# Performance work log

Measured on AMD Instinct MI355X. Metric: run time of the kernel, lower is better.

Reference implementation:

```python
import jax, jax.numpy as jnp
import numpy as np

B, S, D, H = 2, 2048, 1024, 16
HD = D // H


def setup_inputs() -> dict:
    key = jax.random.key(0)
    ks = jax.random.split(key, 9)
    std = 0.02
    return {
        "x": jax.random.normal(ks[0], (B, S, D), dtype=jnp.float32),
        "wq": jax.random.normal(ks[1], (D, D), dtype=jnp.float32) * std,
        "bq": jnp.zeros((D,), dtype=jnp.float32),
        "wk": jax.random.normal(ks[2], (D, D), dtype=jnp.float32) * std,
        "bk": jnp.zeros((D,), dtype=jnp.float32),
        "wv": jax.random.normal(ks[3], (D, D), dtype=jnp.float32) * std,
        "bv": jnp.zeros((D,), dtype=jnp.float32),
        "wo": jax.random.normal(ks[4], (D, D), dtype=jnp.float32) * std,
        "bo": jnp.zeros((D,), dtype=jnp.float32),
    }


def reference(x, wq, bq, wk, bk, wv, bv, wo, bo):
    bsz, seq_len, d_model = x.shape
    # projections: torch Linear computes x @ W.T + b with W of shape (out, in)
    q = (x @ wq.T + bq).reshape(bsz, seq_len, H, HD).transpose(0, 2, 1, 3)  # bhsd
    k = (x @ wk.T + bk).reshape(bsz, seq_len, H, HD).transpose(0, 2, 1, 3)
    v = (x @ wv.T + bv).reshape(bsz, seq_len, H, HD).transpose(0, 2, 1, 3)
    scale = HD ** -0.5
    scores = jnp.einsum("bhqd,bhkd->bhqk", q, k) * scale  # [B,H,S,S]
    causal = jnp.tril(jnp.ones((seq_len, seq_len), dtype=bool))
    scores = jnp.where(causal[None, None], scores, -jnp.inf)
    attn = jax.nn.softmax(scores, axis=-1)
    ctx = jnp.einsum("bhqk,bhkd->bhqd", attn, v)
    ctx = ctx.transpose(0, 2, 1, 3).reshape(bsz, seq_len, d_model)
    return ctx @ wo.T + bo
```

## Files before the change

kernel.cpp:

```cpp
#include <hip/hip_runtime.h>
#include <hip/hip_bf16.h>

#define B_  2
#define S_  2048
#define D_  1024
#define H_  16
#define HD_ 64
#define M_  (B_ * S_)

typedef __bf16 bf16;
typedef __bf16 bf16x4 __attribute__((ext_vector_type(4)));
typedef __bf16 bf16x8 __attribute__((ext_vector_type(8)));
typedef float  f32x4  __attribute__((ext_vector_type(4)));

__device__ __forceinline__ bf16x8 ld8g(const bf16* p) { return *(const bf16x8*)p; }

#define GLL(g, l) __builtin_amdgcn_global_load_lds( \
    (const __attribute__((address_space(1))) void*)(g), \
    (__attribute__((address_space(3))) void*)(l), 16, 0, 0)

__global__ __launch_bounds__(256) void convert_kernel(
    const float* __restrict__ x,  const float* __restrict__ wq,
    const float* __restrict__ wk, const float* __restrict__ wv,
    const float* __restrict__ wo,
    bf16* __restrict__ xb,  bf16* __restrict__ wqb, bf16* __restrict__ wkb,
    bf16* __restrict__ wvb, bf16* __restrict__ wob)
{
    const int seg = blockIdx.y;
    const float* src;
    bf16* dst;
    if (seg < 4)      { src = x  + (long)seg * 1048576; dst = xb  + (long)seg * 1048576; }
    else if (seg == 4){ src = wq; dst = wqb; }
    else if (seg == 5){ src = wk; dst = wkb; }
    else if (seg == 6){ src = wv; dst = wvb; }
    else              { src = wo; dst = wob; }
    const long i = ((long)blockIdx.x * 256 + threadIdx.x) * 8;
    float4 a = *(const float4*)(src + i);
    float4 b = *(const float4*)(src + i + 4);
    bf16x8 r;
    r[0] = (bf16)a.x; r[1] = (bf16)a.y; r[2] = (bf16)a.z; r[3] = (bf16)a.w;
    r[4] = (bf16)b.x; r[5] = (bf16)b.y; r[6] = (bf16)b.z; r[7] = (bf16)b.w;
    *(bf16x8*)(dst + i) = r;
}

__device__ __forceinline__ void gemm_acc_bk32(
    const bf16* __restrict__ A, const bf16* __restrict__ Bt,
    f32x4 (&acc)[4][4])
{
    __shared__ bf16 As[128 * 32];
    __shared__ bf16 Bs[128 * 32];

    const int tid  = threadIdx.x;
    const int wave = tid >> 6;
    const int lane = tid & 63;
    const int quad = lane >> 4;
    const int l15  = lane & 15;
    const int wr   = (wave >> 1) * 64;
    const int wc   = (wave & 1) * 64;
    const int m0   = blockIdx.y * 128;
    const int n0   = blockIdx.x * 128;

    const int sr = wave * 16 + (lane >> 2);
    const int sc = (lane & 3) * 8;
    const bf16* Ag = A  + (long)(m0 + sr) * D_ + sc;
    const bf16* Bg = Bt + (long)(n0 + sr) * D_ + sc;
    bf16* lA = As + wave * 512;
    bf16* lB = Bs + wave * 512;

    for (int k0 = 0; k0 < D_; k0 += 32) {
        __syncthreads();
        GLL(Ag + k0,             lA);
        GLL(Ag + 64 * D_ + k0,   lA + 64 * 32);
        GLL(Bg + k0,             lB);
        GLL(Bg + 64 * D_ + k0,   lB + 64 * 32);
        __syncthreads();

        bf16x8 af[4], bfr[4];
        for (int mi = 0; mi < 4; mi++)
            af[mi] = *(const bf16x8*)&As[(wr + mi * 16 + l15) * 32 + quad * 8];
        for (int ni = 0; ni < 4; ni++)
            bfr[ni] = *(const bf16x8*)&Bs[(wc + ni * 16 + l15) * 32 + quad * 8];

        for (int mi = 0; mi < 4; mi++)
            for (int ni = 0; ni < 4; ni++)
                acc[mi][ni] = __builtin_amdgcn_mfma_f32_16x16x32_bf16(
                    af[mi], bfr[ni], acc[mi][ni], 0, 0, 0);
    }
}

__global__ __launch_bounds__(256) void gemm_qkv(
    const bf16* __restrict__ xb,
    const bf16* __restrict__ wqb, const bf16* __restrict__ wkb, const bf16* __restrict__ wvb,
    const float* __restrict__ bq, const float* __restrict__ bk, const float* __restrict__ bv,
    bf16* __restrict__ qb, bf16* __restrict__ kb, bf16* __restrict__ vt)
{
    const bf16*  Bt   = (blockIdx.z == 0) ? wqb : (blockIdx.z == 1) ? wkb : wvb;
    const float* bias = (blockIdx.z == 0) ? bq  : (blockIdx.z == 1) ? bk  : bv;

    f32x4 acc[4][4] = {};
    gemm_acc_bk32(xb, Bt, acc);

    const int lane = threadIdx.x & 63;
    const int wave = threadIdx.x >> 6;
    const int quad = lane >> 4;
    const int l15  = lane & 15;
    const int wr   = (wave >> 1) * 64;
    const int wc   = (wave & 1) * 64;
    const int m0   = blockIdx.y * 128;
    const int n0   = blockIdx.x * 128;

    if (blockIdx.z < 2) {
        bf16* Cout = (blockIdx.z == 0) ? qb : kb;
        for (int ni = 0; ni < 4; ni++) {
            const int col = n0 + wc + ni * 16 + l15;
            const float bv = bias[col];
            for (int mi = 0; mi < 4; mi++) {
                const int rowb = m0 + wr + mi * 16 + quad * 4;
                for (int r = 0; r < 4; r++)
                    Cout[(long)(rowb + r) * D_ + col] = (bf16)(acc[mi][ni][r] + bv);
            }
        }
    } else {
        for (int ni = 0; ni < 4; ni++) {
            const int col = n0 + wc + ni * 16 + l15;
            const float bv = bias[col];
            const int h = col >> 6, hd = col & (HD_ - 1);
            for (int mi = 0; mi < 4; mi++) {
                const int rowb = m0 + wr + mi * 16 + quad * 4;
                const int b = rowb >> 11;
                const int s0 = rowb & (S_ - 1);
                bf16x4 v4;
                for (int r = 0; r < 4; r++) v4[r] = (bf16)(acc[mi][ni][r] + bv);
                *(bf16x4*)&vt[(((long)(b * H_ + h)) * HD_ + hd) * S_ + s0] = v4;
            }
        }
    }
}

__global__ __launch_bounds__(256) void gemm_out(
    const bf16* __restrict__ cb, const bf16* __restrict__ wob,
    const float* __restrict__ bo, float* __restrict__ out)
{
    f32x4 acc[4][4] = {};
    gemm_acc_bk32(cb, wob, acc);

    const int lane = threadIdx.x & 63;
    const int wave = threadIdx.x >> 6;
    const int quad = lane >> 4;
    const int l15  = lane & 15;
    const int wr   = (wave >> 1) * 64;
    const int wc   = (wave & 1) * 64;
    const int m0   = blockIdx.y * 128;
    const int n0   = blockIdx.x * 128;

    for (int ni = 0; ni < 4; ni++) {
        const int col = n0 + wc + ni * 16 + l15;
        const float bv = bo[col];
        for (int mi = 0; mi < 4; mi++) {
            const int rowb = m0 + wr + mi * 16 + quad * 4;
            for (int r = 0; r < 4; r++)
                out[(long)(rowb + r) * D_ + col] = acc[mi][ni][r] + bv;
        }
    }
}

__global__ __launch_bounds__(512) void attn_kernel(
    const bf16* __restrict__ Q, const bf16* __restrict__ K,
    const bf16* __restrict__ vt, bf16* __restrict__ ctx)
{
    constexpr int LDK = 72;
    __shared__ bf16 Ks[2][64 * LDK];
    __shared__ bf16 Vt[2][64 * LDK];
    __shared__ bf16 Pq[8][16 * LDK];

    const int tid  = threadIdx.x;
    const int wave = tid >> 6;
    const int lane = tid & 63;
    const int quad = lane >> 4;
    const int l15  = lane & 15;
    const int bh   = blockIdx.y;
    const int qt   = (blockIdx.y < 16) ? blockIdx.x : (15 - (int)blockIdx.x);
    const int b    = bh >> 4, h = bh & 15;
    const long base  = ((long)b * S_) * D_ + h * HD_;
    const bf16* Vth  = vt + (long)bh * HD_ * S_;

    const int krow = tid >> 3;
    const int kcol = (tid & 7) * 8;

    const int qw    = qt * 128 + wave * 16;
    const int qrow  = qw + l15;
    const bf16* Qr = Q + base + (long)qrow * D_;
    bf16x8 qf0 = ld8g(&Qr[quad * 8]);
    bf16x8 qf1 = ld8g(&Qr[quad * 8 + 32]);

    float l_i = 0.f;
    f32x4 o_acc[4] = {};

    auto process_tile = [&](int kbase, int buf) {
        if (kbase > qw + 15) return;
        f32x4 sc[4];
        for (int kt = 0; kt < 4; kt++) {
            const bf16* Kr = &Ks[buf][(kt * 16 + l15) * LDK + quad * 8];
            bf16x8 a0 = *(const bf16x8*)Kr;
            bf16x8 a1 = *(const bf16x8*)(Kr + 32);
            f32x4 z = {};
            z = __builtin_amdgcn_mfma_f32_16x16x32_bf16(a0, qf0, z, 0, 0, 0);
            z = __builtin_amdgcn_mfma_f32_16x16x32_bf16(a1, qf1, z, 0, 0, 0);
            sc[kt] = z;
        }
        float sum = 0.f;
        if (kbase + 63 > qw) {
            for (int kt = 0; kt < 4; kt++)
                for (int r = 0; r < 4; r++) {
                    const int k_g = kbase + kt * 16 + quad * 4 + r;
                    const float p = (k_g <= qrow) ? __expf(sc[kt][r] * 0.125f) : 0.f;
                    sc[kt][r] = p;
                    sum += p;
                }
        } else {
            for (int kt = 0; kt < 4; kt++)
                for (int r = 0; r < 4; r++) {
                    const float p = __expf(sc[kt][r] * 0.125f);
                    sc[kt][r] = p;
                    sum += p;
                }
        }
        sum += __shfl_xor(sum, 16, 64);
        sum += __shfl_xor(sum, 32, 64);
        l_i += sum;

        bf16* Pw = &Pq[wave][0];
        for (int kt = 0; kt < 4; kt++) {
            union { uint2 u; bf16 hh[4]; } pk;
            pk.hh[0] = (bf16)sc[kt][0];
            pk.hh[1] = (bf16)sc[kt][1];
            pk.hh[2] = (bf16)sc[kt][2];
            pk.hh[3] = (bf16)sc[kt][3];
            *(uint2*)&Pw[l15 * LDK + kt * 16 + quad * 4] = pk.u;
        }
        __asm__ volatile("s_waitcnt lgkmcnt(0)" ::: "memory");
        bf16x8 pf0 = *(const bf16x8*)&Pw[l15 * LDK + quad * 8];
        bf16x8 pf1 = *(const bf16x8*)&Pw[l15 * LDK + quad * 8 + 32];

        for (int ni = 0; ni < 4; ni++) {
            const bf16* Vr = &Vt[buf][(ni * 16 + l15) * LDK + quad * 8];
            bf16x8 av0 = *(const bf16x8*)Vr;
            bf16x8 av1 = *(const bf16x8*)(Vr + 32);
            o_acc[ni] = __builtin_amdgcn_mfma_f32_16x16x32_bf16(av0, pf0, o_acc[ni], 0, 0, 0);
            o_acc[ni] = __builtin_amdgcn_mfma_f32_16x16x32_bf16(av1, pf1, o_acc[ni], 0, 0, 0);
        }
    };

    bf16x8 kA = ld8g(K + base + (long)krow * D_ + kcol);
    bf16x8 wA = ld8g(Vth + (long)krow * S_ + kcol);
    bf16x8 kB = ld8g(K + base + (long)(64 + krow) * D_ + kcol);
    bf16x8 wB = ld8g(Vth + (long)krow * S_ + 64 + kcol);

    const int njt = 2 * qt + 2;
    for (int j = 0; j < njt; j += 2) {
        __syncthreads();
        *(bf16x8*)&Ks[0][krow * LDK + kcol] = kA;
        *(bf16x8*)&Vt[0][krow * LDK + kcol] = wA;
        *(bf16x8*)&Ks[1][krow * LDK + kcol] = kB;
        *(bf16x8*)&Vt[1][krow * LDK + kcol] = wB;
        if (j + 2 < njt) {
            kA = ld8g(K + base + (long)((j + 2) * 64 + krow) * D_ + kcol);
            wA = ld8g(Vth + (long)krow * S_ + (j + 2) * 64 + kcol);
            kB = ld8g(K + base + (long)((j + 3) * 64 + krow) * D_ + kcol);
            wB = ld8g(Vth + (long)krow * S_ + (j + 3) * 64 + kcol);
        }
        __syncthreads();
        process_tile(j * 64, 0);
        process_tile(j * 64 + 64, 1);
    }

    const float invl = 1.f / l_i;
    bf16* Pw = &Pq[wave][0];
    for (int ni = 0; ni < 4; ni++)
        for (int r = 0; r < 4; r++)
            Pw[l15 * LDK + ni * 16 + quad * 4 + r] = (bf16)(o_acc[ni][r] * invl);
    __asm__ volatile("s_waitcnt lgkmcnt(0)" ::: "memory");
    for (int round = 0; round < 2; round++) {
        const int rowq = (lane >> 3) + round * 8;
        bf16x8 val = *(const bf16x8*)&Pw[rowq * LDK + (lane & 7) * 8];
        const int q_g = qt * 128 + wave * 16 + rowq;
        *(bf16x8*)&ctx[base + (long)q_g * D_ + (lane & 7) * 8] = val;
    }
}

extern "C" void kernel_launch(void* const* d_in, const int* in_sizes, int n_in,
                              void* d_out, int out_size, void* d_ws, size_t ws_size,
                              hipStream_t stream)
{
    const float* x  = (const float*)d_in[0];
    const float* wq = (const float*)d_in[1];
    const float* bq = (const float*)d_in[2];
    const float* wk = (const float*)d_in[3];
    const float* bk = (const float*)d_in[4];
    const float* wv = (const float*)d_in[5];
    const float* bv = (const float*)d_in[6];
    const float* wo = (const float*)d_in[7];
    const float* bo = (const float*)d_in[8];
    float* out = (float*)d_out;

    const long NX = (long)M_ * D_;
    const long NW = (long)D_ * D_;
    bf16* xb  = (bf16*)d_ws;
    bf16* wqb = xb  + NX;
    bf16* wkb = wqb + NW;
    bf16* wvb = wkb + NW;
    bf16* wob = wvb + NW;
    bf16* qb  = wob + NW;
    bf16* kb  = qb  + NX;
    bf16* vt  = kb  + NX;
    bf16* cb  = xb;

    dim3 blk(256, 1, 1);

    convert_kernel<<<dim3(512, 8), blk, 0, stream>>>(
        x, wq, wk, wv, wo, xb, wqb, wkb, wvb, wob);

    gemm_qkv<<<dim3(8, 32, 3), blk, 0, stream>>>(
        xb, wqb, wkb, wvb, bq, bk, bv, qb, kb, vt);

    attn_kernel<<<dim3(16, 32), dim3(512, 1, 1), 0, stream>>>(qb, kb, vt, cb);

    gemm_out<<<dim3(8, 32), blk, 0, stream>>>(cb, wob, bo, out);
}
```

Before: 183.2 us.

## Process two query sub-tiles per wave in attention and shrink output GEMM tile

Result: no change. 185.4 us (+1.2%).

```diff
diff --git a/kernel.cpp b/kernel.cpp
--- a/kernel.cpp
+++ b/kernel.cpp
@@ -141,22 +141,50 @@
     const bf16* __restrict__ cb, const bf16* __restrict__ wob,
     const float* __restrict__ bo, float* __restrict__ out)
 {
-    f32x4 acc[4][4] = {};
-    gemm_acc_bk32(cb, wob, acc);
-
-    const int lane = threadIdx.x & 63;
-    const int wave = threadIdx.x >> 6;
+    __shared__ bf16 As[64 * 32];
+    __shared__ bf16 Bs[128 * 32];
+
+    const int tid  = threadIdx.x;
+    const int wave = tid >> 6;
+    const int lane = tid & 63;
     const int quad = lane >> 4;
     const int l15  = lane & 15;
-    const int wr   = (wave >> 1) * 64;
+    const int wr   = (wave >> 1) * 32;
     const int wc   = (wave & 1) * 64;
-    const int m0   = blockIdx.y * 128;
+    const int m0   = blockIdx.y * 64;
     const int n0   = blockIdx.x * 128;
+
+    const int sr = tid >> 2;
+    const int scg = (tid & 3) * 8;
+    const bf16* Ag = cb  + (long)(m0 + sr) * D_ + scg;
+    const bf16* Bg = wob + (long)(n0 + sr) * D_ + scg;
+    bf16* lA = As + wave * 512;
+    bf16* lB = Bs + wave * 512;
+
+    f32x4 acc[2][4] = {};
+    for (int k0 = 0; k0 < D_; k0 += 32) {
+        __syncthreads();
+        GLL(Ag + k0,            lA);
+        GLL(Bg + k0,            lB);
+        GLL(Bg + 64 * D_ + k0,  lB + 64 * 32);
+        __syncthreads();
+
+        bf16x8 af[2], bfr[4];
+        for (int mi = 0; mi < 2; mi++)
+            af[mi] = *(const bf16x8*)&As[(wr + mi * 16 + l15) * 32 + quad * 8];
+        for (int ni = 0; ni < 4; ni++)
+            bfr[ni] = *(const bf16x8*)&Bs[(wc + ni * 16 + l15) * 32 + quad * 8];
+
+        for (int mi = 0; mi < 2; mi++)
+            for (int ni = 0; ni < 4; ni++)
+                acc[mi][ni] = __builtin_amdgcn_mfma_f32_16x16x32_bf16(
+                    af[mi], bfr[ni], acc[mi][ni], 0, 0, 0);
+    }
 
     for (int ni = 0; ni < 4; ni++) {
         const int col = n0 + wc + ni * 16 + l15;
         const float bv = bo[col];
-        for (int mi = 0; mi < 4; mi++) {
+        for (int mi = 0; mi < 2; mi++) {
             const int rowb = m0 + wr + mi * 16 + quad * 4;
             for (int r = 0; r < 4; r++)
                 out[(long)(rowb + r) * D_ + col] = acc[mi][ni][r] + bv;
@@ -164,14 +192,14 @@
     }
 }
 
-__global__ __launch_bounds__(512) void attn_kernel(
+__global__ __launch_bounds__(256) void attn_kernel(
     const bf16* __restrict__ Q, const bf16* __restrict__ K,
     const bf16* __restrict__ vt, bf16* __restrict__ ctx)
 {
     constexpr int LDK = 72;
     __shared__ bf16 Ks[2][64 * LDK];
     __shared__ bf16 Vt[2][64 * LDK];
-    __shared__ bf16 Pq[8][16 * LDK];
+    __shared__ bf16 Pq[4][32 * LDK];
 
     const int tid  = threadIdx.x;
     const int wave = tid >> 6;
@@ -184,106 +212,170 @@
     const long base  = ((long)b * S_) * D_ + h * HD_;
     const bf16* Vth  = vt + (long)bh * HD_ * S_;
 
-    const int krow = tid >> 3;
-    const int kcol = (tid & 7) * 8;
-
-    const int qw    = qt * 128 + wave * 16;
-    const int qrow  = qw + l15;
-    const bf16* Qr = Q + base + (long)qrow * D_;
-    bf16x8 qf0 = ld8g(&Qr[quad * 8]);
-    bf16x8 qf1 = ld8g(&Qr[quad * 8 + 32]);
-
-    float l_i = 0.f;
-    f32x4 o_acc[4] = {};
+    const int r0 = tid >> 3;
+    const int c0 = (tid & 7) * 8;
+
+    const int qw    = qt * 128 + wave * 32;
+    const int qrow0 = qw + l15;
+    const int qrow1 = qw + 16 + l15;
+    const bf16* Qr0 = Q + base + (long)qrow0 * D_;
+    const bf16* Qr1 = Q + base + (long)qrow1 * D_;
+    bf16x8 qf00 = ld8g(&Qr0[quad * 8]);
+    bf16x8 qf01 = ld8g(&Qr0[quad * 8 + 32]);
+    bf16x8 qf10 = ld8g(&Qr1[quad * 8]);
+    bf16x8 qf11 = ld8g(&Qr1[quad * 8 + 32]);
+
+    float l0 = 0.f, l1 = 0.f;
+    f32x4 o0[4] = {}, o1[4] = {};
 
     auto process_tile = [&](int kbase, int buf) {
-        if (kbase > qw + 15) return;
-        f32x4 sc[4];
+        if (kbase > qw + 31) return;
+        f32x4 s0[4], s1[4];
+        __builtin_amdgcn_s_setprio(1);
+        #pragma unroll
         for (int kt = 0; kt < 4; kt++) {
             const bf16* Kr = &Ks[buf][(kt * 16 + l15) * LDK + quad * 8];
             bf16x8 a0 = *(const bf16x8*)Kr;
             bf16x8 a1 = *(const bf16x8*)(Kr + 32);
-            f32x4 z = {};
-            z = __builtin_amdgcn_mfma_f32_16x16x32_bf16(a0, qf0, z, 0, 0, 0);
-            z = __builtin_amdgcn_mfma_f32_16x16x32_bf16(a1, qf1, z, 0, 0, 0);
-            sc[kt] = z;
-        }
-        float sum = 0.f;
+            f32x4 z0 = {}, z1 = {};
+            z0 = __builtin_amdgcn_mfma_f32_16x16x32_bf16(a0, qf00, z0, 0, 0, 0);
+            z0 = __builtin_amdgcn_mfma_f32_16x16x32_bf16(a1, qf01, z0, 0, 0, 0);
+            z1 = __builtin_amdgcn_mfma_f32_16x16x32_bf16(a0, qf10, z1, 0, 0, 0);
+            z1 = __builtin_amdgcn_mfma_f32_16x16x32_bf16(a1, qf11, z1, 0, 0, 0);
+            s0[kt] = z0; s1[kt] = z1;
+        }
+        __builtin_amdgcn_s_setprio(0);
+
+        float sum0 = 0.f, sum1 = 0.f;
         if (kbase + 63 > qw) {
+            #pragma unroll
             for (int kt = 0; kt < 4; kt++)
+                #pragma unroll
                 for (int r = 0; r < 4; r++) {
                     const int k_g = kbase + kt * 16 + quad * 4 + r;
-                    const float p = (k_g <= qrow) ? __expf(sc[kt][r] * 0.125f) : 0.f;
-                    sc[kt][r] = p;
-                    sum += p;
+                    const float p = (k_g <= qrow0) ? __expf(s0[kt][r] * 0.125f) : 0.f;
+                    s0[kt][r] = p;
+                    sum0 += p;
                 }
         } else {
+            #pragma unroll
             for (int kt = 0; kt < 4; kt++)
+                #pragma unroll
                 for (int r = 0; r < 4; r++) {
-                    const float p = __expf(sc[kt][r] * 0.125f);
-                    sc[kt][r] = p;
-                    sum += p;
+                    const float p = __expf(s0[kt][r] * 0.125f);
+                    s0[kt][r] = p;
+                    sum0 += p;
                 }
         }
-        sum += __shfl_xor(sum, 16, 64);
-        sum += __shfl_xor(sum, 32, 64);
-        l_i += sum;
+        if (kbase + 63 > qw + 16) {
+            #pragma unroll
+            for (int kt = 0; kt < 4; kt++)
+                #pragma unroll
+                for (int r = 0; r < 4; r++) {
+                    const int k_g = kbase + kt * 16 + quad * 4 + r;
+                    const float p = (k_g <= qrow1) ? __expf(s1[kt][r] * 0.125f) : 0.f;
+                    s1[kt][r] = p;
+                    sum1 += p;
+                }
+        } else {
+            #pragma unroll
+            for (int kt = 0; kt < 4; kt++)
+                #pragma unroll
+                for (int r = 0; r < 4; r++) {
+                    const float p = __expf(s1[kt][r] * 0.125f);
+                    s1[kt][r] = p;
+                    sum1 += p;
+                }
+        }
+        sum0 += __shfl_xor(sum0, 16, 64);
+        sum0 += __shfl_xor(sum0, 32, 64);
+        l0 += sum0;
+        sum1 += __shfl_xor(sum1, 16, 64);
+        sum1 += __shfl_xor(sum1, 32, 64);
+        l1 += sum1;
 
         bf16* Pw = &Pq[wave][0];
+        #pragma unroll
         for (int kt = 0; kt < 4; kt++) {
-            union { uint2 u; bf16 hh[4]; } pk;
-            pk.hh[0] = (bf16)sc[kt][0];
-            pk.hh[1] = (bf16)sc[kt][1];
-            pk.hh[2] = (bf16)sc[kt][2];
-            pk.hh[3] = (bf16)sc[kt][3];
-            *(uint2*)&Pw[l15 * LDK + kt * 16 + quad * 4] = pk.u;
+            union { uint2 u; bf16 hh[4]; } p0, p1;
+            p0.hh[0] = (bf16)s0[kt][0]; p0.hh[1] = (bf16)s0[kt][1];
+            p0.hh[2] = (bf16)s0[kt][2]; p0.hh[3] = (bf16)s0[kt][3];
+            p1.hh[0] = (bf16)s1[kt][0]; p1.hh[1] = (bf16)s1[kt][1];
+            p1.hh[2] = (bf16)s1[kt][2]; p1.hh[3] = (bf16)s1[kt][3];
+            *(uint2*)&Pw[l15 * LDK + kt * 16 + quad * 4] = p0.u;
+            *(uint2*)&Pw[(16 + l15) * LDK + kt * 16 + quad * 4] = p1.u;
         }
         __asm__ volatile("s_waitcnt lgkmcnt(0)" ::: "memory");
-        bf16x8 pf0 = *(const bf16x8*)&Pw[l15 * LDK + quad * 8];
-        bf16x8 pf1 = *(const bf16x8*)&Pw[l15 * LDK + quad * 8 + 32];
-
+        bf16x8 pf00 = *(const bf16x8*)&Pw[l15 * LDK + quad * 8];
+        bf16x8 pf01 = *(const bf16x8*)&Pw[l15 * LDK + quad * 8 + 32];
+        bf16x8 pf10 = *(const bf16x8*)&Pw[(16 + l15) * LDK + quad * 8];
+        bf16x8 pf11 = *(const bf16x8*)&Pw[(16 + l15) * LDK + quad * 8 + 32];
+
+        __builtin_amdgcn_s_setprio(1);
+        #pragma unroll
         for (int ni = 0; ni < 4; ni++) {
             const bf16* Vr = &Vt[buf][(ni * 16 + l15) * LDK + quad * 8];
             bf16x8 av0 = *(const bf16x8*)Vr;
             bf16x8 av1 = *(const bf16x8*)(Vr + 32);
-            o_acc[ni] = __builtin_amdgcn_mfma_f32_16x16x32_bf16(av0, pf0, o_acc[ni], 0, 0, 0);
-            o_acc[ni] = __builtin_amdgcn_mfma_f32_16x16x32_bf16(av1, pf1, o_acc[ni], 0, 0, 0);
-        }
+            o0[ni] = __builtin_amdgcn_mfma_f32_16x16x32_bf16(av0, pf00, o0[ni], 0, 0, 0);
+            o0[ni] = __builtin_amdgcn_mfma_f32_16x16x32_bf16(av1, pf01, o0[ni], 0, 0, 0);
+            o1[ni] = __builtin_amdgcn_mfma_f32_16x16x32_bf16(av0, pf10, o1[ni], 0, 0, 0);
+            o1[ni] = __builtin_amdgcn_mfma_f32_16x16x32_bf16(av1, pf11, o1[ni], 0, 0, 0);
+        }
+        __builtin_amdgcn_s_setprio(0);
     };
 
-    bf16x8 kA = ld8g(K + base + (long)krow * D_ + kcol);
-    bf16x8 wA = ld8g(Vth + (long)krow * S_ + kcol);
-    bf16x8 kB = ld8g(K + base + (long)(64 + krow) * D_ + kcol);
-    bf16x8 wB = ld8g(Vth + (long)krow * S_ + 64 + kcol);
+    bf16x8 kA0 = ld8g(K + base + (long)r0 * D_ + c0);
+    bf16x8 kA1 = ld8g(K + base + (long)(r0 + 32) * D_ + c0);
+    bf16x8 wA0 = ld8g(Vth + (long)r0 * S_ + c0);
+    bf16x8 wA1 = ld8g(Vth + (long)(r0 + 32) * S_ + c0);
+    bf16x8 kB0 = ld8g(K + base + (long)(64 + r0) * D_ + c0);
+    bf16x8 kB1 = ld8g(K + base + (long)(64 + r0 + 32) * D_ + c0);
+    bf16x8 wB0 = ld8g(Vth + (long)r0 * S_ + 64 + c0);
+    bf16x8 wB1 = ld8g(Vth + (long)(r0 + 32) * S_ + 64 + c0);
 
     const int njt = 2 * qt + 2;
     for (int j = 0; j < njt; j += 2) {
         __syncthreads();
-        *(bf16x8*)&Ks[0][krow * LDK + kcol] = kA;
-        *(bf16x8*)&Vt[0][krow * LDK + kcol] = wA;
-        *(bf16x8*)&Ks[1][krow * LDK + kcol] = kB;
-        *(bf16x8*)&Vt[1][krow * LDK + kcol] = wB;
+        *(bf16x8*)&Ks[0][r0 * LDK + c0]        = kA0;
+        *(bf16x8*)&Ks[0][(r0 + 32) * LDK + c0] = kA1;
+        *(bf16x8*)&Vt[0][r0 * LDK + c0]        = wA0;
+        *(bf16x8*)&Vt[0][(r0 + 32) * LDK + c0] = wA1;
+        *(bf16x8*)&Ks[1][r0 * LDK + c0]        = kB0;
+        *(bf16x8*)&Ks[1][(r0 + 32) * LDK + c0] = kB1;
+        *(bf16x8*)&Vt[1][r0 * LDK + c0]        = wB0;
+        *(bf16x8*)&Vt[1][(r0 + 32) * LDK + c0] = wB1;
         if (j + 2 < njt) {
-            kA = ld8g(K + base + (long)((j + 2) * 64 + krow) * D_ + kcol);
-            wA = ld8g(Vth + (long)krow * S_ + (j + 2) * 64 + kcol);
-            kB = ld8g(K + base + (long)((j + 3) * 64 + krow) * D_ + kcol);
-            wB = ld8g(Vth + (long)krow * S_ + (j + 3) * 64 + kcol);
+            kA0 = ld8g(K + base + (long)((j + 2) * 64 + r0) * D_ + c0);
+            kA1 = ld8g(K + base + (long)((j + 2) * 64 + r0 + 32) * D_ + c0);
+            wA0 = ld8g(Vth + (long)r0 * S_ + (j + 2) * 64 + c0);
+            wA1 = ld8g(Vth + (long)(r0 + 32) * S_ + (j + 2) * 64 + c0);
+            kB0 = ld8g(K + base + (long)((j + 3) * 64 + r0) * D_ + c0);
+            kB1 = ld8g(K + base + (long)((j + 3) * 64 + r0 + 32) * D_ + c0);
+            wB0 = ld8g(Vth + (long)r0 * S_ + (j + 3) * 64 + c0);
+            wB1 = ld8g(Vth + (long)(r0 + 32) * S_ + (j + 3) * 64 + c0);
         }
         __syncthreads();
         process_tile(j * 64, 0);
         process_tile(j * 64 + 64, 1);
     }
 
-    const float invl = 1.f / l_i;
+    const float inv0 = 1.f / l0;
+    const float inv1 = 1.f / l1;
     bf16* Pw = &Pq[wave][0];
+    #pragma unroll
     for (int ni = 0; ni < 4; ni++)
-        for (int r = 0; r < 4; r++)
-            Pw[l15 * LDK + ni * 16 + quad * 4 + r] = (bf16)(o_acc[ni][r] * invl);
+        #pragma unroll
+        for (int r = 0; r < 4; r++) {
+            Pw[l15 * LDK + ni * 16 + quad * 4 + r]        = (bf16)(o0[ni][r] * inv0);
+            Pw[(16 + l15) * LDK + ni * 16 + quad * 4 + r] = (bf16)(o1[ni][r] * inv1);
+        }
     __asm__ volatile("s_waitcnt lgkmcnt(0)" ::: "memory");
-    for (int round = 0; round < 2; round++) {
+    #pragma unroll
+    for (int round = 0; round < 4; round++) {
         const int rowq = (lane >> 3) + round * 8;
         bf16x8 val = *(const bf16x8*)&Pw[rowq * LDK + (lane & 7) * 8];
-        const int q_g = qt * 128 + wave * 16 + rowq;
+        const int q_g = qt * 128 + wave * 32 + rowq;
         *(bf16x8*)&ctx[base + (long)q_g * D_ + (lane & 7) * 8] = val;
     }
 }
@@ -323,7 +415,7 @@
     gemm_qkv<<<dim3(8, 32, 3), blk, 0, stream>>>(
         xb, wqb, wkb, wvb, bq, bk, bv, qb, kb, vt);
 
-    attn_kernel<<<dim3(16, 32), dim3(512, 1, 1), 0, stream>>>(qb, kb, vt, cb);
-
-    gemm_out<<<dim3(8, 32), blk, 0, stream>>>(cb, wob, bo, out);
-}
+    attn_kernel<<<dim3(16, 32), blk, 0, stream>>>(qb, kb, vt, cb);
+
+    gemm_out<<<dim3(8, 64), blk, 0, stream>>>(cb, wob, bo, out);
+}
```
